# Kernel tuning notes

Hardware: AMD Instinct MI355X
Metric: run time of the kernel (lower is better)

The kernel has to match this reference:

```python
import jax, jax.numpy as jnp
import numpy as np

# -------- configuration (production-scale segmentation head) --------
BS, C, H, W = 8, 256, 96, 96
N = H * W          # nodes in the spanning tree (flattened pixels)
E = N - 1          # spanning-tree edge count
ZETA_G = 0.01      # default zeta_g of Global_APro.forward


def setup_inputs() -> dict:
    key = jax.random.key(0)
    k1, k2 = jax.random.split(key)
    feature_in = jax.random.normal(k1, (BS, 1, H, W), dtype=jnp.float32)
    # scaled so norm2 distances over C=256 channels stay O(1..10)
    embed_in = 0.1 * jax.random.normal(k2, (BS, C, H, W), dtype=jnp.float32)
    # Random spanning trees, one per batch element. Edges are topologically
    # ordered: edge e connects parent=src[e] < child=tgt[e]=e+1, so processing
    # edges in order is a valid root->leaf sweep (and reversed is leaf->root).
    rng = np.random.default_rng(0)
    trees = []
    children = np.arange(1, N, dtype=np.int32)
    for _ in range(BS):
        parents = np.floor(rng.random(E) * np.arange(1, N)).astype(np.int32)
        trees.append(np.stack([parents, children], axis=1))
    tree = jnp.asarray(np.stack(trees, axis=0))  # [BS, E, 2] int32
    return {"feature_in": feature_in, "embed_in": embed_in, "tree": tree}


def _gp_single(f, wgt, src, tgt):
    """Global affinity propagation (tree filter) on one tree.
    Computes out_i = sum_j A_ij f_j / sum_j A_ij with A_ij = prod of edge
    affinities along the unique tree path i->j, via the classic two-pass DP.
    f: [N], wgt/src/tgt: [E] (edges topologically ordered, parent=src).
    """
    ones = jnp.ones_like(f)

    def up(carry, xs):                 # leaf -> root aggregation
        S, Z = carry
        s, t, we = xs
        S = S.at[s].add(we * S[t])
        Z = Z.at[s].add(we * Z[t])
        return (S, Z), None

    (S, Z), _ = jax.lax.scan(up, (f, ones), (src, tgt, wgt), reverse=True)

    def down(carry, xs):               # root -> leaf propagation
        F, G = carry
        s, t, we = xs
        F = F.at[t].set(we * F[s] + (1.0 - we * we) * F[t])
        G = G.at[t].set(we * G[s] + (1.0 - we * we) * G[t])
        return (F, G), None

    (F, G), _ = jax.lax.scan(down, (S, Z), (src, tgt, wgt))
    return F / G


def reference(feature_in, embed_in, tree):
    bs, c, h, w = embed_in.shape
    n = h * w
    emb = embed_in.reshape(bs, c, n)               # [bs, c, N]
    src = tree[:, :, 0]                            # [bs, E]
    tgt = tree[:, :, 1]                            # [bs, E]
    # gather node embeddings along tree edges (get_true_index)
    gather = jax.vmap(lambda e, i: e[:, i])        # [c, N], [E] -> [c, E]
    src_node = gather(emb, src)                    # [bs, c, E]
    tgt_node = gather(emb, tgt)                    # [bs, c, E]
    diff = src_node - tgt_node
    dist = jnp.sum(diff * diff, axis=1)            # norm2_distance -> [bs, E]
    wgt = jnp.exp(-ZETA_G * dist)                  # edge affinity
    f = feature_in.reshape(bs, n)                  # [bs, N]
    out = jax.vmap(_gp_single)(f, wgt, src, tgt)   # [bs, N]
    return out.reshape(bs, 1, h, w)
```

## Files before the change

kernel.cpp:

```cpp
#include <hip/hip_runtime.h>
#include <hip/hip_bf16.h>
#include <hip/hip_fp16.h>

#define BS 8
#define C  256
#define N  9216
#define E  9215
#define MAXD 128
#define LVL_STRIDE 192
#define NARROW 64
#define NGT 31
#define NBLK (BS + BS * NGT)

typedef __attribute__((address_space(1))) const void GVoid;
typedef __attribute__((address_space(3))) void LVoid;

__global__ __launch_bounds__(1024) void setup_kernel(const float* __restrict__ emb,
                                                     const int* __restrict__ tree,
                                                     float* __restrict__ distG,
                                                     int* __restrict__ uparr,
                                                     int* __restrict__ lvlOff) {
    __shared__ int P[N];
    __shared__ int U[N];
    __shared__ int cnt8[MAXD * 8];
    __shared__ int tot[MAXD];
    __shared__ int sc1[MAXD];
    __shared__ int off[MAXD + 1];
    __shared__ int maxd_sh;
    const int tid = threadIdx.x;

    if (blockIdx.x >= BS) {
        const int wb = blockIdx.x - BS;
        const int b  = wb & 7;
        const int g  = wb >> 3;
        const int c0  = (g < 8) ? g * 9 : 72 + (g - 8) * 8;
        const int cpg = (g < 8) ? 9 : 8;
        const int wave = tid >> 6, lane = tid & 63;

        float* cur = (float*)P;
        float* nxt = (float*)U;

        int se[9];
        #pragma unroll
        for (int k = 0; k < 9; ++k) {
            int e = tid + k * 1024;
            se[k] = (e < E) ? tree[((size_t)b * E + e) * 2] : 0;
        }
        float acc[9];
        #pragma unroll
        for (int k = 0; k < 9; ++k) acc[k] = 0.f;

        const float* rowbase = emb + ((size_t)b * C + c0) * N;
        for (int chk = wave; chk < 36; chk += 16)
            __builtin_amdgcn_global_load_lds(
                (GVoid*)(rowbase + chk * 256 + lane * 4),
                (LVoid*)(cur + chk * 256), 16, 0, 0);
        __syncthreads();

        for (int cc = 0; cc < cpg; ++cc) {
            if (cc + 1 < cpg) {
                const float* src = rowbase + (size_t)(cc + 1) * N;
                for (int chk = wave; chk < 36; chk += 16)
                    __builtin_amdgcn_global_load_lds(
                        (GVoid*)(src + chk * 256 + lane * 4),
                        (LVoid*)(nxt + chk * 256), 16, 0, 0);
            }
            #pragma unroll
            for (int k = 0; k < 9; ++k) {
                int e = tid + k * 1024;
                if (e < E) {
                    float d = cur[se[k]] - cur[e + 1];
                    acc[k] += d * d;
                }
            }
            __syncthreads();
            float* t = cur; cur = nxt; nxt = t;
        }
        #pragma unroll
        for (int k = 0; k < 9; ++k) {
            int e = tid + k * 1024;
            if (e < E) atomicAdd(&distG[(size_t)b * N + e], acc[k]);
        }
        return;
    }

    const int b = blockIdx.x;
    const int* tb = tree + b * E * 2;

    for (int t = tid; t < N; t += 1024)
        P[t] = (t == 0) ? 0 : (tb[(t - 1) * 2] | (1 << 16));
    for (int i = tid; i < MAXD * 8; i += 1024) cnt8[i] = 0;
    if (tid == 0) maxd_sh = 1;
    __syncthreads();

    for (int r = 0; r < 3; ++r) {
        for (int t = tid; t < N; t += 1024) {
            int p = P[t];
            int a = p & 0xffff;
            if (a == 0) U[t] = p;
            else {
                int pa = P[a];
                U[t] = (pa & 0xffff) | (((p >> 16) + (pa >> 16)) << 16);
            }
        }
        __syncthreads();
        for (int t = tid; t < N; t += 1024) {
            int p = U[t];
            int a = p & 0xffff;
            if (a == 0) P[t] = p;
            else {
                int pa = U[a];
                P[t] = (pa & 0xffff) | (((p >> 16) + (pa >> 16)) << 16);
            }
        }
        __syncthreads();
    }

    for (int t = 1 + tid; t < N; t += 1024) {
        int d = P[t] >> 16;
        atomicAdd(&cnt8[d * 8 + (tid >> 7)], 1);
    }
    __syncthreads();

    for (int d = tid; d < MAXD; d += 1024) {
        int s = 0;
        #pragma unroll
        for (int k = 0; k < 8; ++k) {
            int v = cnt8[d * 8 + k];
            cnt8[d * 8 + k] = s;
            s += v;
        }
        tot[d] = s;
        if (s > 0) atomicMax(&maxd_sh, d);
    }
    __syncthreads();

    {
        int* src = tot; int* dst = sc1;
        for (int step = 1; step < MAXD; step <<= 1) {
            for (int d = tid; d < MAXD; d += 1024)
                dst[d] = src[d] + ((d >= step) ? src[d - step] : 0);
            __syncthreads();
            int* tmp = src; src = dst; dst = tmp;
        }
        for (int d = tid; d < MAXD; d += 1024) off[d + 1] = src[d];
        if (tid == 0) off[0] = 0;
    }
    __syncthreads();

    if (tid == 0) {
        int md = maxd_sh;
        int lo = 0;
        while (lo < md && off[lo + 2] - off[lo + 1] <= NARROW) ++lo;
        int hi = md + 1;
        while (hi > lo + 1 && off[hi] - off[hi - 1] <= NARROW) --hi;
        lvlOff[b * LVL_STRIDE + 129] = md;
        lvlOff[b * LVL_STRIDE + 130] = lo;
        lvlOff[b * LVL_STRIDE + 131] = hi;
    }
    for (int t = 1 + tid; t < N; t += 1024) {
        int d = P[t] >> 16;
        int idx = atomicAdd(&cnt8[d * 8 + (tid >> 7)], 1);
        int slot = off[d] + idx;
        int p = tb[(t - 1) * 2];
        U[slot] = t | (p << 16);
    }
    __syncthreads();

    for (int i = tid; i < E; i += 1024) uparr[b * N + i] = U[i];
    for (int i = tid; i <= MAXD; i += 1024) lvlOff[b * LVL_STRIDE + i] = off[i];
}

__device__ __forceinline__ void up_edge(float2* V, const int2& ew) {
    int t = ew.x & 0xffff, p = ew.x >> 16;
    float w = __int_as_float(ew.y);
    float2 vt = V[t];
    atomicAdd(&V[p].x, w * vt.x);
    atomicAdd(&V[p].y, w * vt.y);
}

__device__ __forceinline__ void down_edge(float2* V, const int2& ew) {
    int t = ew.x & 0xffff, s = ew.x >> 16;
    float w = __int_as_float(ew.y);
    float2 vs = V[s], vt = V[t];
    float c = 1.f - w * w;
    V[t] = make_float2(w * vs.x + c * vt.x, w * vs.y + c * vt.y);
}

__global__ __launch_bounds__(1024) void dp_kernel(const float* __restrict__ feat,
                                                  const int* __restrict__ lvlOff,
                                                  const int* __restrict__ uparr,
                                                  const float* __restrict__ distG,
                                                  float* __restrict__ out) {
    const int b = blockIdx.x;
    const int tid = threadIdx.x;
    __shared__ float2 V[N];
    __shared__ int2 TSW[N];
    __shared__ int off[MAXD + 1];
    __shared__ int meta[3];

    for (int i = tid; i <= MAXD; i += 1024) off[i] = lvlOff[b * LVL_STRIDE + i];
    if (tid < 3) meta[tid] = lvlOff[b * LVL_STRIDE + 129 + tid];

    float* dScr = (float*)V;
    const float* dG = distG + b * N;
    for (int i = tid; i < N; i += 1024) dScr[i] = dG[i];
    __syncthreads();

    const int* uA = uparr + b * N;
    for (int i = tid; i < E; i += 1024) {
        int ts = uA[i];
        float ds = dScr[(ts & 0xffff) - 1];
        TSW[i] = make_int2(ts, __float_as_int(__expf(-0.01f * ds)));
    }
    __syncthreads();

    for (int i = tid; i < N; i += 1024)
        V[i] = make_float2(feat[b * N + i], 1.0f);
    __syncthreads();
    const int maxd = meta[0], loE = meta[1], hiS = meta[2];

    if (tid < 64) {
        for (int lev = maxd; lev >= hiS; --lev) {
            int s0 = off[lev], s1 = off[lev + 1];
            for (int i = s0 + tid; i < s1; i += 64) up_edge(V, TSW[i]);
            __threadfence_block();
        }
    }
    __syncthreads();
    for (int lev = hiS - 1; lev > loE; --lev) {
        int s0 = off[lev], s1 = off[lev + 1];
        for (int i = s0 + tid; i < s1; i += 1024) up_edge(V, TSW[i]);
        __syncthreads();
    }
    if (tid < 64) {
        for (int lev = loE; lev >= 1; --lev) {
            int s0 = off[lev], s1 = off[lev + 1];
            for (int i = s0 + tid; i < s1; i += 64) up_edge(V, TSW[i]);
            __threadfence_block();
        }
    }
    __syncthreads();

    if (tid < 64) {
        for (int lev = 1; lev <= loE; ++lev) {
            int s0 = off[lev], s1 = off[lev + 1];
            for (int i = s0 + tid; i < s1; i += 64) down_edge(V, TSW[i]);
            __threadfence_block();
        }
    }
    __syncthreads();
    for (int lev = loE + 1; lev < hiS; ++lev) {
        int s0 = off[lev], s1 = off[lev + 1];
        for (int i = s0 + tid; i < s1; i += 1024) down_edge(V, TSW[i]);
        __syncthreads();
    }
    if (tid < 64) {
        for (int lev = hiS; lev <= maxd; ++lev) {
            int s0 = off[lev], s1 = off[lev + 1];
            for (int i = s0 + tid; i < s1; i += 64) down_edge(V, TSW[i]);
            __threadfence_block();
        }
    }
    __syncthreads();

    for (int i = tid; i < N; i += 1024) {
        float2 v = V[i];
        out[b * N + i] = v.x / v.y;
    }
}

extern "C" void kernel_launch(void* const* d_in, const int* in_sizes, int n_in,
                              void* d_out, int out_size, void* d_ws, size_t ws_size,
                              hipStream_t stream) {
    const float* feat = (const float*)d_in[0];
    const float* emb  = (const float*)d_in[1];
    const int*   tree = (const int*)d_in[2];
    float* out = (float*)d_out;

    const size_t BN = (size_t)BS * N;
    float* distG  = (float*)d_ws;
    int*   uparr  = (int*)((char*)d_ws + BN * 4);
    int*   lvlOff = (int*)((char*)d_ws + BN * 8);

    hipMemsetAsync(distG, 0, BN * sizeof(float), stream);
    setup_kernel<<<NBLK, 1024, 0, stream>>>(emb, tree, distG, uparr, lvlOff);
    dp_kernel<<<BS, 1024, 0, stream>>>(feat, lvlOff, uparr, distG, out);
}
```

Before: 156.7 us.

## Replace level-wise down sweep with pointer-jumping scan over tree ancestors

Rewrites the root-to-leaf propagation as a parallel pointer-jumping composition of affine maps. Each node starts from (1-w^2)·value and repeatedly doubles its ancestor reach over six rounds, one barrier pair per round. This removes the serial per-level sweeps and the narrow 64-thread phases for deep levels. The fixed six rounds assume tree depth stays within 64, which the code does not check against its level limit of 128.

```diff
diff --git a/kernel.cpp b/kernel.cpp
--- a/kernel.cpp
+++ b/kernel.cpp
@@ -179,14 +179,6 @@
     atomicAdd(&V[p].y, w * vt.y);
 }
 
-__device__ __forceinline__ void down_edge(float2* V, const int2& ew) {
-    int t = ew.x & 0xffff, s = ew.x >> 16;
-    float w = __int_as_float(ew.y);
-    float2 vs = V[s], vt = V[t];
-    float c = 1.f - w * w;
-    V[t] = make_float2(w * vs.x + c * vt.x, w * vs.y + c * vt.y);
-}
-
 __global__ __launch_bounds__(1024) void dp_kernel(const float* __restrict__ feat,
                                                   const int* __restrict__ lvlOff,
                                                   const int* __restrict__ uparr,
@@ -242,27 +234,70 @@
     }
     __syncthreads();
 
-    if (tid < 64) {
-        for (int lev = 1; lev <= loE; ++lev) {
-            int s0 = off[lev], s1 = off[lev + 1];
-            for (int i = s0 + tid; i < s1; i += 64) down_edge(V, TSW[i]);
-            __threadfence_block();
-        }
-    }
-    __syncthreads();
-    for (int lev = loE + 1; lev < hiS; ++lev) {
-        int s0 = off[lev], s1 = off[lev + 1];
-        for (int i = s0 + tid; i < s1; i += 1024) down_edge(V, TSW[i]);
-        __syncthreads();
-    }
-    if (tid < 64) {
-        for (int lev = hiS; lev <= maxd; ++lev) {
-            int s0 = off[lev], s1 = off[lev + 1];
-            for (int i = s0 + tid; i < s1; i += 64) down_edge(V, TSW[i]);
-            __threadfence_block();
-        }
-    }
-    __syncthreads();
+    int   own_t[9], own_p[9];
+    float own_a[9];
+    float2 own_b[9];
+
+    #pragma unroll
+    for (int k = 0; k < 9; ++k) {
+        int e = tid + k * 1024;
+        if (e < E) {
+            int2 ew = TSW[e];
+            own_t[k] = ew.x & 0xffff;
+            own_p[k] = ew.x >> 16;
+            own_a[k] = __int_as_float(ew.y);
+        } else { own_t[k] = 0; own_p[k] = 0; own_a[k] = 0.f; }
+    }
+    __syncthreads();
+
+    #pragma unroll
+    for (int k = 0; k < 9; ++k) {
+        int e = tid + k * 1024;
+        if (e < E) {
+            int t = own_t[k];
+            float w = own_a[k], c = 1.f - w * w;
+            float2 s = V[t];
+            float2 bb = make_float2(c * s.x, c * s.y);
+            own_b[k] = bb;
+            V[t] = bb;
+            TSW[t] = make_int2(own_p[k], __float_as_int(w));
+        }
+    }
+    if (tid == 0) TSW[0] = make_int2(0, 0);
+    __syncthreads();
+
+    for (int r = 0; r < 6; ++r) {
+        int   pp[9];
+        float pa[9];
+        float2 pb[9];
+        #pragma unroll
+        for (int k = 0; k < 9; ++k) {
+            int e = tid + k * 1024;
+            if (e < E) {
+                int p = own_p[k];
+                int2 d = TSW[p];
+                pp[k] = d.x;
+                pa[k] = __int_as_float(d.y);
+                pb[k] = V[p];
+            } else { pp[k] = 0; pa[k] = 0.f; pb[k] = make_float2(0.f, 0.f); }
+        }
+        __syncthreads();
+        #pragma unroll
+        for (int k = 0; k < 9; ++k) {
+            int e = tid + k * 1024;
+            if (e < E) {
+                float a = own_a[k];
+                own_b[k].x = a * pb[k].x + own_b[k].x;
+                own_b[k].y = a * pb[k].y + own_b[k].y;
+                own_a[k] = a * pa[k];
+                own_p[k] = pp[k];
+                int t = own_t[k];
+                V[t] = own_b[k];
+                TSW[t] = make_int2(own_p[k], __float_as_int(own_a[k]));
+            }
+        }
+        __syncthreads();
+    }
 
     for (int i = tid; i < N; i += 1024) {
         float2 v = V[i];
```

New measurement: 165.3 us. 1.05x slower.
